# Kernel tuning notes

Hardware: AMD Instinct MI355X
Metric: run time of the kernel (lower is better)

Reference implementation:

```python
import jax, jax.numpy as jnp
import numpy as np

N, E, H, L = 50000, 800000, 96, 4

def _gelu(x):
    return jax.nn.gelu(x, approximate=False)

def _mlp2(x, w1, b1, w2, b2):
    # Linear -> GELU -> (Dropout=identity in eval) -> Linear
    return _gelu(x @ w1 + b1) @ w2 + b2

def setup_inputs() -> dict:
    key = jax.random.key(0)
    ks = jax.random.split(key, 40)
    p = lambda k, s: jax.random.normal(k, s, jnp.float32) * 0.05
    inp = {
        'x': jax.random.normal(ks[0], (N, 6), jnp.float32),
        'edge_index': jax.random.randint(ks[1], (2, E), 0, N, jnp.int64),
        'edge_attr': jax.random.normal(ks[2], (E, 8), jnp.float32),
        # node encoder
        'ne_w1': p(ks[3], (6, H)), 'ne_b1': p(ks[4], (H,)),
        'ne_w2': p(ks[5], (H, H)), 'ne_b2': p(ks[6], (H,)),
        # edge encoder
        'ee_w1': p(ks[7], (8, H)), 'ee_b1': p(ks[8], (H,)),
        'ee_w2': p(ks[9], (H, H)), 'ee_b2': p(ks[10], (H,)),
        # per-layer message-passing MLPs (stacked over L)
        'mp_ew1': p(ks[11], (L, 3 * H, H)), 'mp_eb1': p(ks[12], (L, H)),
        'mp_ew2': p(ks[13], (L, H, H)),     'mp_eb2': p(ks[14], (L, H)),
        'mp_nw1': p(ks[15], (L, 2 * H, H)), 'mp_nb1': p(ks[16], (L, H)),
        'mp_nw2': p(ks[17], (L, H, H)),     'mp_nb2': p(ks[18], (L, H)),
        # node saliency head
        'nh_w1': p(ks[19], (H, H)), 'nh_b1': p(ks[20], (H,)),
        'nh_w2': p(ks[21], (H, 1)), 'nh_b2': p(ks[22], (1,)),
        # edge clustering head
        'eh_w1': p(ks[23], (3 * H, H)), 'eh_b1': p(ks[24], (H,)),
        'eh_w2': p(ks[25], (H, 1)),     'eh_b2': p(ks[26], (1,)),
    }
    return inp

def _forward(x, edge_attr, ne_w1, ne_b1, ne_w2, ne_b2, ee_w1, ee_b1, ee_w2, ee_b2,
             mp_ew1, mp_eb1, mp_ew2, mp_eb2, mp_nw1, mp_nb1, mp_nw2, mp_nb2,
             nh_w1, nh_b1, nh_w2, nh_b2, eh_w1, eh_b1, eh_w2, eh_b2, edge_index):
    src, dst = edge_index[0], edge_index[1]
    h = _mlp2(x, ne_w1, ne_b1, ne_w2, ne_b2)                 # [N,H]
    e = _mlp2(edge_attr, ee_w1, ee_b1, ee_w2, ee_b2)         # [E,H]
    for l in range(L):
        # edge update: residual MLP over [h_src, h_dst, e]
        m = jnp.concatenate([h[src], h[dst], e], axis=-1)    # [E,3H]
        e = e + _mlp2(m, mp_ew1[l], mp_eb1[l], mp_ew2[l], mp_eb2[l])
        # node update: residual MLP over [h, sum of incoming edge states]
        agg = jax.ops.segment_sum(e, dst, num_segments=N)    # [N,H]
        h = h + _mlp2(jnp.concatenate([h, agg], axis=-1), mp_nw1[l], mp_nb1[l], mp_nw2[l], mp_nb2[l])
    edge_logits = _mlp2(jnp.concatenate([h[src], h[dst], e], axis=-1), eh_w1, eh_b1, eh_w2, eh_b2)[:, 0]
    node_logits = _mlp2(h, nh_w1, nh_b1, nh_w2, nh_b2)[:, 0]
    return edge_logits, node_logits

def reference(x, edge_index, edge_attr, ne_w1, ne_b1, ne_w2, ne_b2, ee_w1, ee_b1, ee_w2, ee_b2,
              mp_ew1, mp_eb1, mp_ew2, mp_eb2, mp_nw1, mp_nb1, mp_nw2, mp_nb2,
              nh_w1, nh_b1, nh_w2, nh_b2, eh_w1, eh_b1, eh_w2, eh_b2):
    return _forward(x, edge_attr, ne_w1, ne_b1, ne_w2, ne_b2, ee_w1, ee_b1, ee_w2, ee_b2,
                    mp_ew1, mp_eb1, mp_ew2, mp_eb2, mp_nw1, mp_nb1, mp_nw2, mp_nb2,
                    nh_w1, nh_b1, nh_w2, nh_b2, eh_w1, eh_b1, eh_w2, eh_b2, edge_index)
```

## Files before the change

kernel.cpp:

```cpp
#include <hip/hip_runtime.h>
#include <hip/hip_bf16.h>
#include <math.h>


typedef __attribute__((ext_vector_type(8))) short short8;
typedef __attribute__((ext_vector_type(4))) float f32x4;

#define MFMA(a, b, c) __builtin_amdgcn_mfma_f32_16x16x32_bf16((a), (b), (c), 0, 0, 0)
#define WSTR 112

__device__ __forceinline__ float bf2f(ushort u) {
    union { uint i; float f; } v; v.i = ((uint)u) << 16; return v.f;
}
__device__ __forceinline__ ushort f2bf(float f) {
    union { float f; uint i; } v; v.f = f;
    uint b = v.i;
    return (ushort)((b + 0x7FFFu + ((b >> 16) & 1u)) >> 16);
}
__device__ __forceinline__ float gelu_f(float x) {
    return 0.5f * x * (1.0f + erff(x * 0.70710678118654752440f));
}
__device__ __forceinline__ short8 ld8(const ushort* p) { return *(const short8*)p; }
__device__ __forceinline__ ushort cvt_elem(const void* p, size_t j, int f32) {
    return f32 ? f2bf(((const float*)p)[j]) : ((const ushort*)p)[j];
}
template <int NT>
__device__ __forceinline__ void stageW(ushort* dst, const ushort* src, int t) {
    for (int i = t; i < 1152; i += NT) {
        int row = i / 12, ch = i - row * 12;
        ((short8*)dst)[row * 14 + ch] = ((const short8*)src)[i];
    }
}

__global__ __launch_bounds__(256) void detect_kernel(
    const ushort* __restrict__ X, const uint* __restrict__ IDX, int* __restrict__ flags)
{
    __shared__ int cnt[2];
    if (threadIdx.x == 0) { cnt[0] = 0; cnt[1] = 0; }
    __syncthreads();
    int plaus = 0;
    for (int i = threadIdx.x; i < 2048; i += 256) {
        float v = fabsf(bf2f(X[i]));
        if (v > 1e-3f && v < 100.f) plaus++;
    }
    atomicAdd(&cnt[0], plaus);
    int nz = 0;
    for (int i = threadIdx.x; i < 1024; i += 256)
        if (IDX[2 * i + 1] != 0) nz++;
    atomicAdd(&cnt[1], nz);
    __syncthreads();
    if (threadIdx.x == 0) {
        flags[0] = (cnt[0] < 1843) ? 1 : 0;
        flags[1] = (cnt[1] == 0) ? 1 : 0;
    }
}

struct SPk { const void* src[16]; int off[17]; };
__global__ __launch_bounds__(256) void smalls_kernel(SPk p, ushort* __restrict__ dst,
                                                     const int* __restrict__ flags) {
    int f = flags[0];
    for (int i = threadIdx.x; i < 3650; i += 256) {
        int e = 0;
        while (e < 15 && i >= p.off[e + 1]) e++;
        dst[i] = cvt_elem(p.src[e], (size_t)(i - p.off[e]), f);
    }
}

struct TPk { const void* base[34]; int eloff[34]; };
__global__ __launch_bounds__(256) void transpose_k(TPk p, ushort* __restrict__ dst,
                                                   const int* __restrict__ flags) {
    int f = flags[0];
    int m = blockIdx.x;
    const void* s = p.base[m];
    size_t off = (size_t)p.eloff[m];
    ushort* d = dst + (size_t)m * 9216;
    for (int i = threadIdx.x; i < 9216; i += 256) {
        int n = i / 96, k = i - n * 96;
        d[i] = cvt_elem(s, off + (size_t)k * 96 + n, f);
    }
}

__global__ __launch_bounds__(256) void idx_convert(
    const int* __restrict__ eidx, int* __restrict__ s32, int* __restrict__ d32,
    const int* __restrict__ flags, int E)
{
    int f = flags[1];
    for (size_t i = (size_t)blockIdx.x * 256 + threadIdx.x; i < (size_t)E;
         i += (size_t)gridDim.x * 256) {
        s32[i] = f ? eidx[2 * i] : eidx[i];
        d32[i] = f ? eidx[2 * ((size_t)E + i)] : eidx[(size_t)E + i];
    }
}

__global__ __launch_bounds__(256) void xe_convert(
    const void* __restrict__ xin, const void* __restrict__ ein,
    ushort* __restrict__ xb, ushort* __restrict__ eb,
    const int* __restrict__ flags, size_t nx, size_t ne)
{
    int f = flags[0];
    size_t total = nx + ne;
    for (size_t i = (size_t)blockIdx.x * 256 + threadIdx.x; i < total;
         i += (size_t)gridDim.x * 256) {
        if (i < nx) xb[i] = cvt_elem(xin, i, f);
        else        eb[i - nx] = cvt_elem(ein, i - nx, f);
    }
}

__global__ __launch_bounds__(256) void hist_kernel(const int* __restrict__ d32,
                                                   int* __restrict__ cnt, int E) {
    for (size_t i = (size_t)blockIdx.x * 256 + threadIdx.x; i < (size_t)E;
         i += (size_t)gridDim.x * 256)
        atomicAdd(&cnt[d32[i]], 1);
}

__global__ __launch_bounds__(1024) void prefix_kernel(int* __restrict__ cnt,
                                                      int* __restrict__ rowptr,
                                                      int N, int E) {
    __shared__ int part[1024];
    int t = threadIdx.x;
    int chunk = (N + 1023) / 1024;
    int b = t * chunk, e = b + chunk; if (e > N) e = N;
    int s = 0;
    for (int i = b; i < e; i++) s += cnt[i];
    part[t] = s;
    __syncthreads();
    for (int off = 1; off < 1024; off <<= 1) {
        int v = (t >= off) ? part[t - off] : 0;
        __syncthreads();
        part[t] += v;
        __syncthreads();
    }
    int run = part[t] - s;
    for (int i = b; i < e; i++) {
        int c = cnt[i];
        rowptr[i] = run;
        cnt[i] = run;
        run += c;
    }
    if (t == 1023) rowptr[N] = E;
}

__global__ __launch_bounds__(256) void scatter_kernel(
    const int* __restrict__ s32, const int* __restrict__ d32,
    int* __restrict__ cursor, int* __restrict__ ss, int* __restrict__ ds,
    int* __restrict__ eid, int E)
{
    for (size_t i = (size_t)blockIdx.x * 256 + threadIdx.x; i < (size_t)E;
         i += (size_t)gridDim.x * 256) {
        int d = d32[i];
        int pos = atomicAdd(&cursor[d], 1);
        ss[pos] = s32[i];
        ds[pos] = d;
        eid[pos] = (int)i;
    }
}

template <int K, bool WF32>
__global__ __launch_bounds__(256) void encoder_kernel(
    const ushort* __restrict__ X, const ushort* __restrict__ W1,
    const ushort* __restrict__ B1, const ushort* __restrict__ W2t,
    const ushort* __restrict__ B2, ushort* __restrict__ OutB,
    float* __restrict__ OutF, const int* __restrict__ EID, int R)
{
    __shared__ __align__(16) ushort sW2[96 * WSTR];
    __shared__ float sW1[K * 96];
    __shared__ float sb1[96], sb2[96];
    __shared__ __align__(16) ushort gscr[4][16 * WSTR];
    int t = threadIdx.x;
    stageW<256>(sW2, W2t, t);
    for (int i = t; i < K * 96; i += 256) sW1[i] = bf2f(W1[i]);
    if (t < 96) { sb1[t] = bf2f(B1[t]); sb2[t] = bf2f(B2[t]); }
    __syncthreads();

    const int wave = t >> 6, lane = t & 63, lr = lane & 15, cg = lane >> 4, lk = cg * 8;
    int rbase = blockIdx.x * 64 + wave * 16;

    float wf[K][6];
#pragma unroll
    for (int k = 0; k < K; k++)
#pragma unroll
        for (int n = 0; n < 6; n++) wf[k][n] = sW1[k * 96 + n * 16 + lr];

    ushort* g = gscr[wave];
#pragma unroll
    for (int j = 0; j < 4; j++) {
        int r = rbase + cg * 4 + j;
        int rc = r < R ? r : R - 1;
        int rx = EID ? EID[rc] : rc;
        float xr[K];
        const uint* xu = (const uint*)(X + (size_t)rx * K);
#pragma unroll
        for (int q = 0; q < K / 2; q++) {
            uint u = xu[q];
            xr[2 * q] = bf2f((ushort)u); xr[2 * q + 1] = bf2f((ushort)(u >> 16));
        }
#pragma unroll
        for (int n = 0; n < 6; n++) {
            float v = sb1[n * 16 + lr];
#pragma unroll
            for (int k = 0; k < K; k++) v += xr[k] * wf[k][n];
            g[(cg * 4 + j) * WSTR + n * 16 + lr] = f2bf(gelu_f(v));
        }
    }
    __syncthreads();

    const ushort* grow = g + lr * WSTR + lk;
    short8 a0 = ld8(grow), a1 = ld8(grow + 32), a2 = ld8(grow + 64);
    f32x4 acc[6];
#pragma unroll
    for (int n = 0; n < 6; n++) {
        f32x4 z = {0.f, 0.f, 0.f, 0.f}; acc[n] = z;
        const ushort* wb = sW2 + (n * 16 + lr) * WSTR + lk;
        acc[n] = MFMA(a0, ld8(wb), acc[n]);
        acc[n] = MFMA(a1, ld8(wb + 32), acc[n]);
        acc[n] = MFMA(a2, ld8(wb + 64), acc[n]);
    }
#pragma unroll
    for (int j = 0; j < 4; j++) {
        int r = rbase + cg * 4 + j;
        if (r < R) {
#pragma unroll
            for (int n = 0; n < 6; n++) {
                int c = n * 16 + lr;
                float v = acc[n][j] + sb2[c];
                OutB[(size_t)r * 96 + c] = f2bf(v);
                if constexpr (WF32) OutF[(size_t)r * 96 + c] = v;
            }
        }
    }
}

__global__ __launch_bounds__(256) void gemm_dual_kernel(
    const ushort* __restrict__ A, const ushort* __restrict__ W1t,
    const ushort* __restrict__ W2t, ushort* __restrict__ O1,
    ushort* __restrict__ O2, int R)
{
    __shared__ __align__(16) ushort sW1[96 * WSTR], sW2[96 * WSTR];
    int t = threadIdx.x;
    stageW<256>(sW1, W1t, t);
    stageW<256>(sW2, W2t, t);
    __syncthreads();
    const int wave = t >> 6, lane = t & 63, lr = lane & 15, cg = lane >> 4, lk = cg * 8;
    int rbase = blockIdx.x * 64 + wave * 16;
    int ra = rbase + lr; if (ra > R - 1) ra = R - 1;
    const ushort* arow = A + (size_t)ra * 96 + lk;
    short8 a0 = ld8(arow), a1 = ld8(arow + 32), a2 = ld8(arow + 64);
    f32x4 acc1[6], acc2[6];
#pragma unroll
    for (int n = 0; n < 6; n++) {
        f32x4 z = {0.f, 0.f, 0.f, 0.f}; acc1[n] = z; acc2[n] = z;
        const ushort* w1 = sW1 + (n * 16 + lr) * WSTR + lk;
        const ushort* w2 = sW2 + (n * 16 + lr) * WSTR + lk;
        acc1[n] = MFMA(a0, ld8(w1), acc1[n]);
        acc1[n] = MFMA(a1, ld8(w1 + 32), acc1[n]);
        acc1[n] = MFMA(a2, ld8(w1 + 64), acc1[n]);
        acc2[n] = MFMA(a0, ld8(w2), acc2[n]);
        acc2[n] = MFMA(a1, ld8(w2 + 32), acc2[n]);
        acc2[n] = MFMA(a2, ld8(w2 + 64), acc2[n]);
    }
#pragma unroll
    for (int j = 0; j < 4; j++) {
        int r = rbase + cg * 4 + j;
        if (r < R) {
#pragma unroll
            for (int n = 0; n < 6; n++) {
                int c = n * 16 + lr;
                O1[(size_t)r * 96 + c] = f2bf(acc1[n][j]);
                O2[(size_t)r * 96 + c] = f2bf(acc2[n][j]);
            }
        }
    }
}

__global__ __launch_bounds__(512) void edge_layer_kernel(
    ushort* __restrict__ Eio,
    const ushort* __restrict__ HA, const ushort* __restrict__ HB,
    const int* __restrict__ SRC, const int* __restrict__ DST,
    const ushort* __restrict__ W1t, const ushort* __restrict__ B1,
    const ushort* __restrict__ W2t, const ushort* __restrict__ B2,
    int ntiles, int Etot)
{
    __shared__ __align__(16) ushort sW1[96 * WSTR], sW2[96 * WSTR];
    __shared__ __align__(16) ushort gscr[8][16 * WSTR];
    __shared__ float sb1[96], sb2[96];
    int t = threadIdx.x;
    stageW<512>(sW1, W1t, t);
    stageW<512>(sW2, W2t, t);
    if (t < 96) { sb1[t] = bf2f(B1[t]); sb2[t] = bf2f(B2[t]); }
    __syncthreads();
    const int wave = t >> 6, lane = t & 63, lr = lane & 15, cg = lane >> 4, lk = cg * 8;
    ushort* g = gscr[wave];

    for (int tile = blockIdx.x; tile < ntiles; tile += gridDim.x) {
        int rbase = tile * 128 + wave * 16;
        int ra = rbase + lr; if (ra > Etot - 1) ra = Etot - 1;
        const ushort* arow = Eio + (size_t)ra * 96 + lk;
        short8 a0 = ld8(arow), a1 = ld8(arow + 32), a2 = ld8(arow + 64);
        f32x4 acc[6];
#pragma unroll
        for (int n = 0; n < 6; n++) {
            f32x4 z = {0.f, 0.f, 0.f, 0.f}; acc[n] = z;
            const ushort* wb = sW1 + (n * 16 + lr) * WSTR + lk;
            acc[n] = MFMA(a0, ld8(wb), acc[n]);
            acc[n] = MFMA(a1, ld8(wb + 32), acc[n]);
            acc[n] = MFMA(a2, ld8(wb + 64), acc[n]);
        }
        int s4[4], d4[4];
#pragma unroll
        for (int j = 0; j < 4; j++) {
            int r = rbase + cg * 4 + j; if (r > Etot - 1) r = Etot - 1;
            s4[j] = SRC[r]; d4[j] = DST[r];
        }
#pragma unroll
        for (int j = 0; j < 4; j++) {
            const ushort* pa = HA + (size_t)s4[j] * 96;
            const ushort* pb = HB + (size_t)d4[j] * 96;
            int rl = cg * 4 + j;
#pragma unroll
            for (int n = 0; n < 6; n++) {
                int c = n * 16 + lr;
                float v = acc[n][j] + bf2f(pa[c]) + bf2f(pb[c]) + sb1[c];
                g[rl * WSTR + c] = f2bf(gelu_f(v));
            }
        }
        __syncthreads();
        const ushort* grow = g + lr * WSTR + lk;
        short8 b0 = ld8(grow), b1v = ld8(grow + 32), b2v = ld8(grow + 64);
        f32x4 acc2[6];
#pragma unroll
        for (int n = 0; n < 6; n++) {
            f32x4 z = {0.f, 0.f, 0.f, 0.f}; acc2[n] = z;
            const ushort* wb = sW2 + (n * 16 + lr) * WSTR + lk;
            acc2[n] = MFMA(b0, ld8(wb), acc2[n]);
            acc2[n] = MFMA(b1v, ld8(wb + 32), acc2[n]);
            acc2[n] = MFMA(b2v, ld8(wb + 64), acc2[n]);
        }
#pragma unroll
        for (int j = 0; j < 4; j++) {
            int r = rbase + cg * 4 + j;
            if (r < Etot) {
                ushort* erow = Eio + (size_t)r * 96;
#pragma unroll
                for (int n = 0; n < 6; n++) {
                    int c = n * 16 + lr;
                    float v = acc2[n][j] + sb2[c] + bf2f(erow[c]);
                    erow[c] = f2bf(v);
                }
            }
        }
        __syncthreads();
    }
}

template <bool HF32>
__global__ __launch_bounds__(256) void node_layer_kernel(
    float* __restrict__ HF, ushort* __restrict__ HBF,
    const ushort* __restrict__ EB, const int* __restrict__ ROWPTR,
    const ushort* __restrict__ W1at, const ushort* __restrict__ W1bt,
    const ushort* __restrict__ B1, const ushort* __restrict__ W2t,
    const ushort* __restrict__ B2, int R)
{
    __shared__ __align__(16) ushort sWa[96 * WSTR], sWb[96 * WSTR], sW2[96 * WSTR];
    __shared__ __align__(16) ushort gscr[4][16 * WSTR];
    __shared__ float sb1[96], sb2[96];
    int t = threadIdx.x;
    stageW<256>(sWa, W1at, t);
    stageW<256>(sWb, W1bt, t);
    stageW<256>(sW2, W2t, t);
    if (t < 96) { sb1[t] = bf2f(B1[t]); sb2[t] = bf2f(B2[t]); }
    __syncthreads();
    const int wave = t >> 6, lane = t & 63, lr = lane & 15, cg = lane >> 4, lk = cg * 8;
    int rbase = blockIdx.x * 64 + wave * 16;
    int ra = rbase + lr; if (ra > R - 1) ra = R - 1;
    const ushort* hrow = HBF + (size_t)ra * 96 + lk;
    short8 a0 = ld8(hrow), a1 = ld8(hrow + 32), a2 = ld8(hrow + 64);

    float ag[24];
#pragma unroll
    for (int i = 0; i < 24; i++) ag[i] = 0.f;
    int beg = ROWPTR[ra], end = ROWPTR[ra + 1];
    for (int k = beg; k < end; k++) {
        const ushort* er = EB + (size_t)k * 96 + lk;
        short8 e0 = ld8(er), e1 = ld8(er + 32), e2 = ld8(er + 64);
#pragma unroll
        for (int i = 0; i < 8; i++) {
            ag[i]      += bf2f((ushort)e0[i]);
            ag[8 + i]  += bf2f((ushort)e1[i]);
            ag[16 + i] += bf2f((ushort)e2[i]);
        }
    }
    short8 g0, g1, g2;
#pragma unroll
    for (int i = 0; i < 8; i++) {
        g0[i] = (short)f2bf(ag[i]);
        g1[i] = (short)f2bf(ag[8 + i]);
        g2[i] = (short)f2bf(ag[16 + i]);
    }

    f32x4 acc[6];
#pragma unroll
    for (int n = 0; n < 6; n++) {
        f32x4 z = {0.f, 0.f, 0.f, 0.f}; acc[n] = z;
        const ushort* wa = sWa + (n * 16 + lr) * WSTR + lk;
        const ushort* wb = sWb + (n * 16 + lr) * WSTR + lk;
        acc[n] = MFMA(a0, ld8(wa), acc[n]);
        acc[n] = MFMA(a1, ld8(wa + 32), acc[n]);
        acc[n] = MFMA(a2, ld8(wa + 64), acc[n]);
        acc[n] = MFMA(g0, ld8(wb), acc[n]);
        acc[n] = MFMA(g1, ld8(wb + 32), acc[n]);
        acc[n] = MFMA(g2, ld8(wb + 64), acc[n]);
    }
    ushort* g = gscr[wave];
#pragma unroll
    for (int j = 0; j < 4; j++) {
        int rl = cg * 4 + j;
#pragma unroll
        for (int n = 0; n < 6; n++) {
            int c = n * 16 + lr;
            g[rl * WSTR + c] = f2bf(gelu_f(acc[n][j] + sb1[c]));
        }
    }
    __syncthreads();
    const ushort* grow = g + lr * WSTR + lk;
    short8 b0 = ld8(grow), b1v = ld8(grow + 32), b2v = ld8(grow + 64);
    f32x4 acc2[6];
#pragma unroll
    for (int n = 0; n < 6; n++) {
        f32x4 z = {0.f, 0.f, 0.f, 0.f}; acc2[n] = z;
        const ushort* wb = sW2 + (n * 16 + lr) * WSTR + lk;
        acc2[n] = MFMA(b0, ld8(wb), acc2[n]);
        acc2[n] = MFMA(b1v, ld8(wb + 32), acc2[n]);
        acc2[n] = MFMA(b2v, ld8(wb + 64), acc2[n]);
    }
#pragma unroll
    for (int j = 0; j < 4; j++) {
        int r = rbase + cg * 4 + j;
        if (r < R) {
#pragma unroll
            for (int n = 0; n < 6; n++) {
                int c = n * 16 + lr;
                size_t idx = (size_t)r * 96 + c;
                float base;
                if constexpr (HF32) base = HF[idx]; else base = bf2f(HBF[idx]);
                float v = base + acc2[n][j] + sb2[c];
                if constexpr (HF32) HF[idx] = v;
                HBF[idx] = f2bf(v);
            }
        }
    }
}

template <bool GATHER>
__global__ __launch_bounds__(256) void head_kernel(
    const ushort* __restrict__ Arows,
    const ushort* __restrict__ HA, const ushort* __restrict__ HB,
    const int* __restrict__ SRC, const int* __restrict__ DST,
    const ushort* __restrict__ W1t, const ushort* __restrict__ B1,
    const ushort* __restrict__ W2v, const ushort* __restrict__ B2,
    float* __restrict__ Out, const int* __restrict__ EID, int R)
{
    __shared__ __align__(16) ushort sW1[96 * WSTR];
    __shared__ float sb1[96], sw2[96];
    __shared__ float sb2s;
    int t = threadIdx.x;
    stageW<256>(sW1, W1t, t);
    if (t < 96) { sb1[t] = bf2f(B1[t]); sw2[t] = bf2f(W2v[t]); }
    if (t == 0) sb2s = bf2f(B2[0]);
    __syncthreads();
    const int wave = t >> 6, lane = t & 63, lr = lane & 15, cg = lane >> 4, lk = cg * 8;
    int rbase = blockIdx.x * 64 + wave * 16;
    int ra = rbase + lr; if (ra > R - 1) ra = R - 1;
    const ushort* arow = Arows + (size_t)ra * 96 + lk;
    short8 a0 = ld8(arow), a1 = ld8(arow + 32), a2 = ld8(arow + 64);
    f32x4 acc[6];
#pragma unroll
    for (int n = 0; n < 6; n++) {
        f32x4 z = {0.f, 0.f, 0.f, 0.f}; acc[n] = z;
        const ushort* wb = sW1 + (n * 16 + lr) * WSTR + lk;
        acc[n] = MFMA(a0, ld8(wb), acc[n]);
        acc[n] = MFMA(a1, ld8(wb + 32), acc[n]);
        acc[n] = MFMA(a2, ld8(wb + 64), acc[n]);
    }
    float s[4] = {0.f, 0.f, 0.f, 0.f};
#pragma unroll
    for (int j = 0; j < 4; j++) {
        int r = rbase + cg * 4 + j;
        int rc = r < R ? r : R - 1;
        const ushort* pa = nullptr; const ushort* pb = nullptr;
        if constexpr (GATHER) {
            pa = HA + (size_t)SRC[rc] * 96;
            pb = HB + (size_t)DST[rc] * 96;
        }
#pragma unroll
        for (int n = 0; n < 6; n++) {
            int c = n * 16 + lr;
            float v = acc[n][j] + sb1[c];
            if constexpr (GATHER) v += bf2f(pa[c]) + bf2f(pb[c]);
            s[j] += gelu_f(v) * sw2[c];
        }
    }
#pragma unroll
    for (int m = 1; m < 16; m <<= 1) {
#pragma unroll
        for (int j = 0; j < 4; j++) s[j] += __shfl_xor(s[j], m, 16);
    }
    if (lr == 0) {
#pragma unroll
        for (int j = 0; j < 4; j++) {
            int r = rbase + cg * 4 + j;
            if (r < R) {
                int ro = EID ? EID[r] : r;
                Out[ro] = s[j] + sb2s;
            }
        }
    }
}

extern "C" void kernel_launch(void* const* d_in, const int* in_sizes, int n_in,
                              void* d_out, int out_size, void* d_ws, size_t ws_size,
                              hipStream_t stream)
{
    (void)n_in; (void)out_size;
    const int N = in_sizes[0] / 6;
    const int E = in_sizes[2] / 8;

    auto a256 = [](size_t b) { return (b + 255) & ~(size_t)255; };
    const size_t sz_flags = 256;
    const size_t sz_wt    = a256((size_t)34 * 9216 * 2);
    const size_t sz_sm    = a256(3650 * 2);
    const size_t sz_hbf   = a256((size_t)N * 96 * 2);
    const size_t sz_ebuf  = a256((size_t)E * 96 * 2);
    const size_t sz_idx   = a256((size_t)E * 4);
    const size_t sz_np    = a256((size_t)(N + 1) * 4);
    const size_t sz_xbf   = a256((size_t)N * 6 * 2);
    const size_t sz_eabf  = a256((size_t)E * 8 * 2);
    const size_t sz_hf    = a256((size_t)N * 96 * 4);

    const size_t need_base   = sz_flags + sz_wt + sz_sm + 3 * sz_hbf + sz_ebuf
                             + 2 * sz_np + 3 * sz_idx;
    const size_t need_copies = need_base + 2 * sz_idx + sz_xbf + sz_eabf;
    const size_t need_full   = need_copies + sz_hf;
    int mode = (ws_size >= need_full) ? 0 : (ws_size >= need_copies) ? 1 : 2;
    const bool hf32 = (mode == 0), copies = (mode <= 1);

    char* ws = (char*)d_ws;
    size_t off = 0;
    auto alloc = [&](size_t bytes) -> void* { void* p = ws + off; off += bytes; return p; };
    int*    flags  = (int*)alloc(sz_flags);
    ushort* wtpool = (ushort*)alloc(sz_wt);
    ushort* smalls = (ushort*)alloc(sz_sm);
    ushort* h_bf   = (ushort*)alloc(sz_hbf);
    ushort* hA     = (ushort*)alloc(sz_hbf);
    ushort* hB     = (ushort*)alloc(sz_hbf);
    ushort* ebuf   = (ushort*)alloc(sz_ebuf);
    int*    cnt    = (int*)alloc(sz_np);
    int*    rowptr = (int*)alloc(sz_np);
    int*    src_s  = (int*)alloc(sz_idx);
    int*    dst_s  = (int*)alloc(sz_idx);
    int*    eid    = (int*)alloc(sz_idx);
    const int* eidx = (const int*)d_in[1];
    int*    src32 = copies ? (int*)alloc(sz_idx) : (int*)eidx;
    int*    dst32 = copies ? (int*)alloc(sz_idx) : (int*)(eidx + E);
    ushort* x_bf  = copies ? (ushort*)alloc(sz_xbf)  : (ushort*)d_in[0];
    ushort* ea_bf = copies ? (ushort*)alloc(sz_eabf) : (ushort*)d_in[2];
    float*  h_f32 = hf32 ? (float*)alloc(sz_hf) : nullptr;

    SPk sp;
    const int soff[17] = {0, 576, 672, 768, 1536, 1632, 1728, 2112, 2496, 2880,
                          3264, 3360, 3456, 3552, 3648, 3649, 3650};
    for (int i = 0; i < 17; i++) sp.off[i] = soff[i];
    sp.src[0]  = d_in[3];   sp.src[1]  = d_in[4];   sp.src[2]  = d_in[6];
    sp.src[3]  = d_in[7];   sp.src[4]  = d_in[8];   sp.src[5]  = d_in[10];
    sp.src[6]  = d_in[12];  sp.src[7]  = d_in[14];  sp.src[8]  = d_in[16];
    sp.src[9]  = d_in[18];  sp.src[10] = d_in[20];  sp.src[11] = d_in[21];
    sp.src[12] = d_in[24];  sp.src[13] = d_in[25];  sp.src[14] = d_in[22];
    sp.src[15] = d_in[26];
    auto SM = [&](int o) { return smalls + o; };

    TPk tp; int q = 0;
    tp.base[q] = d_in[5];  tp.eloff[q++] = 0;
    tp.base[q] = d_in[9];  tp.eloff[q++] = 0;
    for (int l = 0; l < 4; l++) {
        tp.base[q] = d_in[11]; tp.eloff[q++] = l * 27648;
        tp.base[q] = d_in[11]; tp.eloff[q++] = l * 27648 + 9216;
        tp.base[q] = d_in[11]; tp.eloff[q++] = l * 27648 + 18432;
        tp.base[q] = d_in[13]; tp.eloff[q++] = l * 9216;
        tp.base[q] = d_in[15]; tp.eloff[q++] = l * 18432;
        tp.base[q] = d_in[15]; tp.eloff[q++] = l * 18432 + 9216;
        tp.base[q] = d_in[17]; tp.eloff[q++] = l * 9216;
    }
    tp.base[q] = d_in[23]; tp.eloff[q++] = 0;
    tp.base[q] = d_in[23]; tp.eloff[q++] = 9216;
    tp.base[q] = d_in[23]; tp.eloff[q++] = 18432;
    tp.base[q] = d_in[19]; tp.eloff[q++] = 0;
    auto WT = [&](int i) { return wtpool + (size_t)i * 9216; };

    const int nblkN = (N + 63) / 64;
    const int nblkE = (E + 63) / 64;
    const int ntilE128 = (E + 127) / 128;

    detect_kernel<<<1, 256, 0, stream>>>((const ushort*)d_in[0], (const uint*)d_in[1], flags);
    smalls_kernel<<<1, 256, 0, stream>>>(sp, smalls, flags);
    transpose_k<<<34, 256, 0, stream>>>(tp, wtpool, flags);
    if (copies) {
        idx_convert<<<1024, 256, 0, stream>>>(eidx, src32, dst32, flags, E);
        xe_convert<<<2048, 256, 0, stream>>>(d_in[0], d_in[2], x_bf, ea_bf, flags,
                                             (size_t)N * 6, (size_t)E * 8);
    }
    hipMemsetAsync(cnt, 0, (size_t)(N + 1) * 4, stream);
    hist_kernel<<<1024, 256, 0, stream>>>(dst32, cnt, E);
    prefix_kernel<<<1, 1024, 0, stream>>>(cnt, rowptr, N, E);
    scatter_kernel<<<1024, 256, 0, stream>>>(src32, dst32, cnt, src_s, dst_s, eid, E);

    if (hf32)
        encoder_kernel<6, true><<<nblkN, 256, 0, stream>>>(x_bf, SM(0), SM(576), WT(0), SM(672), h_bf, h_f32, nullptr, N);
    else
        encoder_kernel<6, false><<<nblkN, 256, 0, stream>>>(x_bf, SM(0), SM(576), WT(0), SM(672), h_bf, nullptr, nullptr, N);
    encoder_kernel<8, false><<<nblkE, 256, 0, stream>>>(ea_bf, SM(768), SM(1536), WT(1), SM(1632), ebuf, nullptr, eid, E);

    for (int l = 0; l < 4; l++) {
        int b = 2 + l * 7;
        gemm_dual_kernel<<<nblkN, 256, 0, stream>>>(h_bf, WT(b + 0), WT(b + 1), hA, hB, N);
        int egrid = ntilE128 < 2048 ? ntilE128 : 2048;
        edge_layer_kernel<<<egrid, 512, 0, stream>>>(
            ebuf, hA, hB, src_s, dst_s, WT(b + 2), SM(1728 + l * 96),
            WT(b + 3), SM(2112 + l * 96), ntilE128, E);
        if (hf32)
            node_layer_kernel<true><<<nblkN, 256, 0, stream>>>(
                h_f32, h_bf, ebuf, rowptr, WT(b + 4), WT(b + 5), SM(2496 + l * 96),
                WT(b + 6), SM(2880 + l * 96), N);
        else
            node_layer_kernel<false><<<nblkN, 256, 0, stream>>>(
                nullptr, h_bf, ebuf, rowptr, WT(b + 4), WT(b + 5), SM(2496 + l * 96),
                WT(b + 6), SM(2880 + l * 96), N);
    }

    gemm_dual_kernel<<<nblkN, 256, 0, stream>>>(h_bf, WT(30), WT(31), hA, hB, N);
    float* out = (float*)d_out;
    head_kernel<true><<<nblkE, 256, 0, stream>>>(
        ebuf, hA, hB, src_s, dst_s, WT(32), SM(3456), SM(3552), SM(3649), out, eid, E);
    head_kernel<false><<<nblkN, 256, 0, stream>>>(
        h_bf, nullptr, nullptr, nullptr, nullptr, WT(33), SM(3264), SM(3360), SM(3648), out + E, nullptr, N);
}
```

Before: 1.517 ms.

## Keep edge MLP hidden activations in registers via transposed MFMA and lane shuffles

The edge layer kernel now computes the first GEMM transposed (weights as A operand), so each lane holds four consecutive hidden columns of one edge row. It gathers HA/HB rows with vectorized 8-byte loads per lane instead of scalar loads for four rows. The GELU outputs are packed to bf16 and redistributed into the second MFMA's A-fragment layout with wave shuffles, removing the per-wave LDS scratch buffer and both block-wide __syncthreads per tile. This cuts LDS traffic, block synchronisation and shared memory use, which may raise occupancy. In exchange it adds shuffle instructions and depends on the MFMA lane-mapping being exactly right.

New measurement: 1.524 ms. About the same (+0.5%).

```diff
diff --git a/kernel.cpp b/kernel.cpp
--- a/kernel.cpp
+++ b/kernel.cpp
@@ -281,7 +281,6 @@
     int ntiles, int Etot)
 {
     __shared__ __align__(16) ushort sW1[96 * WSTR], sW2[96 * WSTR];
-    __shared__ __align__(16) ushort gscr[8][16 * WSTR];
     __shared__ float sb1[96], sb2[96];
     int t = threadIdx.x;
     stageW<512>(sW1, W1t, t);
@@ -289,51 +288,73 @@
     if (t < 96) { sb1[t] = bf2f(B1[t]); sb2[t] = bf2f(B2[t]); }
     __syncthreads();
     const int wave = t >> 6, lane = t & 63, lr = lane & 15, cg = lane >> 4, lk = cg * 8;
-    ushort* g = gscr[wave];
+    const int srcA = ((cg & 1) * 2) * 16 + lr;
+    const int srcB = srcA + 16;
+    const bool hi = (cg >> 1) != 0;
 
     for (int tile = blockIdx.x; tile < ntiles; tile += gridDim.x) {
         int rbase = tile * 128 + wave * 16;
         int ra = rbase + lr; if (ra > Etot - 1) ra = Etot - 1;
         const ushort* arow = Eio + (size_t)ra * 96 + lk;
         short8 a0 = ld8(arow), a1 = ld8(arow + 32), a2 = ld8(arow + 64);
-        f32x4 acc[6];
+
+        f32x4 accT[6];
 #pragma unroll
         for (int n = 0; n < 6; n++) {
-            f32x4 z = {0.f, 0.f, 0.f, 0.f}; acc[n] = z;
+            f32x4 z = {0.f, 0.f, 0.f, 0.f}; accT[n] = z;
             const ushort* wb = sW1 + (n * 16 + lr) * WSTR + lk;
-            acc[n] = MFMA(a0, ld8(wb), acc[n]);
-            acc[n] = MFMA(a1, ld8(wb + 32), acc[n]);
-            acc[n] = MFMA(a2, ld8(wb + 64), acc[n]);
-        }
-        int s4[4], d4[4];
-#pragma unroll
-        for (int j = 0; j < 4; j++) {
-            int r = rbase + cg * 4 + j; if (r > Etot - 1) r = Etot - 1;
-            s4[j] = SRC[r]; d4[j] = DST[r];
-        }
-#pragma unroll
-        for (int j = 0; j < 4; j++) {
-            const ushort* pa = HA + (size_t)s4[j] * 96;
-            const ushort* pb = HB + (size_t)d4[j] * 96;
-            int rl = cg * 4 + j;
-#pragma unroll
-            for (int n = 0; n < 6; n++) {
-                int c = n * 16 + lr;
-                float v = acc[n][j] + bf2f(pa[c]) + bf2f(pb[c]) + sb1[c];
-                g[rl * WSTR + c] = f2bf(gelu_f(v));
-            }
-        }
-        __syncthreads();
-        const ushort* grow = g + lr * WSTR + lk;
-        short8 b0 = ld8(grow), b1v = ld8(grow + 32), b2v = ld8(grow + 64);
+            accT[n] = MFMA(ld8(wb), a0, accT[n]);
+            accT[n] = MFMA(ld8(wb + 32), a1, accT[n]);
+            accT[n] = MFMA(ld8(wb + 64), a2, accT[n]);
+        }
+
+        int s0 = SRC[ra], d0 = DST[ra];
+        const ushort* pa = HA + (size_t)s0 * 96 + cg * 4;
+        const ushort* pb = HB + (size_t)d0 * 96 + cg * 4;
+        uint pk[12];
+#pragma unroll
+        for (int n = 0; n < 6; n++) {
+            uint2 ua = *(const uint2*)(pa + n * 16);
+            uint2 ub = *(const uint2*)(pb + n * 16);
+            const float* b1p = sb1 + n * 16 + cg * 4;
+            float g0f = gelu_f(accT[n][0] + bf2f((ushort)ua.x) + bf2f((ushort)ub.x) + b1p[0]);
+            float g1f = gelu_f(accT[n][1] + bf2f((ushort)(ua.x >> 16)) + bf2f((ushort)(ub.x >> 16)) + b1p[1]);
+            float g2f = gelu_f(accT[n][2] + bf2f((ushort)ua.y) + bf2f((ushort)ub.y) + b1p[2]);
+            float g3f = gelu_f(accT[n][3] + bf2f((ushort)(ua.y >> 16)) + bf2f((ushort)(ub.y >> 16)) + b1p[3]);
+            pk[2 * n]     = (uint)f2bf(g0f) | ((uint)f2bf(g1f) << 16);
+            pk[2 * n + 1] = (uint)f2bf(g2f) | ((uint)f2bf(g3f) << 16);
+        }
+
+        short8 frag[3];
+#pragma unroll
+        for (int m = 0; m < 3; m++) {
+            int nlo = 2 * m, nhi = 2 * m + 1;
+            uint alo0 = (uint)__shfl((int)pk[2 * nlo],     srcA, 64);
+            uint alo1 = (uint)__shfl((int)pk[2 * nlo + 1], srcA, 64);
+            uint ahi0 = (uint)__shfl((int)pk[2 * nhi],     srcA, 64);
+            uint ahi1 = (uint)__shfl((int)pk[2 * nhi + 1], srcA, 64);
+            uint blo0 = (uint)__shfl((int)pk[2 * nlo],     srcB, 64);
+            uint blo1 = (uint)__shfl((int)pk[2 * nlo + 1], srcB, 64);
+            uint bhi0 = (uint)__shfl((int)pk[2 * nhi],     srcB, 64);
+            uint bhi1 = (uint)__shfl((int)pk[2 * nhi + 1], srcB, 64);
+            uint d0w = hi ? ahi0 : alo0;
+            uint d1w = hi ? ahi1 : alo1;
+            uint d2w = hi ? bhi0 : blo0;
+            uint d3w = hi ? bhi1 : blo1;
+            frag[m][0] = (short)(d0w & 0xffff); frag[m][1] = (short)(d0w >> 16);
+            frag[m][2] = (short)(d1w & 0xffff); frag[m][3] = (short)(d1w >> 16);
+            frag[m][4] = (short)(d2w & 0xffff); frag[m][5] = (short)(d2w >> 16);
+            frag[m][6] = (short)(d3w & 0xffff); frag[m][7] = (short)(d3w >> 16);
+        }
+
         f32x4 acc2[6];
 #pragma unroll
         for (int n = 0; n < 6; n++) {
             f32x4 z = {0.f, 0.f, 0.f, 0.f}; acc2[n] = z;
             const ushort* wb = sW2 + (n * 16 + lr) * WSTR + lk;
-            acc2[n] = MFMA(b0, ld8(wb), acc2[n]);
-            acc2[n] = MFMA(b1v, ld8(wb + 32), acc2[n]);
-            acc2[n] = MFMA(b2v, ld8(wb + 64), acc2[n]);
+            acc2[n] = MFMA(frag[0], ld8(wb), acc2[n]);
+            acc2[n] = MFMA(frag[1], ld8(wb + 32), acc2[n]);
+            acc2[n] = MFMA(frag[2], ld8(wb + 64), acc2[n]);
         }
 #pragma unroll
         for (int j = 0; j < 4; j++) {
@@ -348,7 +369,6 @@
                 }
             }
         }
-        __syncthreads();
     }
 }
 
```
